# Optimization experiments

Measured on AMD Instinct MI355X. Metric: run time of the kernel, lower is better.

Reference implementation:

```python
import jax, jax.numpy as jnp
import numpy as np
import math
from jax import lax


def quick_gelu(v):
    return v * jax.nn.sigmoid(1.702 * v)


def setup_inputs() -> dict:
    key = jax.random.key(0)
    k0, k1, k2, k3 = jax.random.split(key, 4)
    B, N, C, dim = 64, 1024, 768, 8
    x = jax.random.normal(k0, (B, N, C), dtype=jnp.float32)
    # adapter_down: Linear(C -> dim), xavier-ish init
    Wd = jax.random.normal(k1, (C, dim), dtype=jnp.float32) * (1.0 / math.sqrt(C))
    bd = jnp.zeros((dim,), dtype=jnp.float32)
    # adapter_conv: Conv2d(dim, dim, 3, stride=1, pad=1), HWIO layout
    Wc = jax.random.normal(k2, (3, 3, dim, dim), dtype=jnp.float32) * (1.0 / math.sqrt(9 * dim))
    bc = jnp.zeros((dim,), dtype=jnp.float32)
    # adapter_up: Linear(dim -> C); torch inits this to zeros, but use small
    # random values so the output/gradients are non-trivial for testing.
    Wu = jax.random.normal(k3, (dim, C), dtype=jnp.float32) * 0.02
    bu = jnp.zeros((C,), dtype=jnp.float32)
    return {"x": x, "Wd": Wd, "bd": bd, "Wc": Wc, "bc": bc, "Wu": Wu, "bu": bu}


def reference(x, Wd, bd, Wc, bc, Wu, bu):
    B, N, C = x.shape
    H = int(math.isqrt(N))  # N is a static perfect square (patch grid)
    dim = Wd.shape[1]
    # down projection: [B, N, C] -> [B, N, dim]
    x_down = jnp.einsum("bnc,cd->bnd", x, Wd) + bd
    # reshape to NHWC patch grid, activate, 3x3 same-pad conv
    x_patch = quick_gelu(x_down.reshape(B, H, H, dim))
    x_patch = lax.conv_general_dilated(
        x_patch, Wc, window_strides=(1, 1), padding="SAME",
        dimension_numbers=("NHWC", "HWIO", "NHWC")) + bc
    # flatten back, activate (dropout = identity in eval), up projection
    x_down = quick_gelu(x_patch.reshape(B, N, dim))
    x_up = jnp.einsum("bnd,dc->bnc", x_down, Wu) + bu
    return x_up
```

## Files before the change

### kernel.cpp

```cpp
#include <hip/hip_runtime.h>

#define B_  64
#define N_  1024
#define H_  32
#define C_  768
#define D_  8

__device__ __forceinline__ float qgelu(float v) {
    return v / (1.0f + __expf(-1.702f * v));
}

__device__ __forceinline__ void async_cp16(const float* gp, float* lp) {
    __builtin_amdgcn_global_load_lds(
        (const __attribute__((address_space(1))) void*)gp,
        (__attribute__((address_space(3))) void*)lp, 16, 0, 0);
}

__device__ __forceinline__ void reduce8(float* acc, int lane) {
    {
        const bool hi = lane & 1;
#pragma unroll
        for (int j = 0; j < 4; ++j) {
            const float a = acc[j], b = acc[j + 4];
            acc[j] = hi ? b : a;
            acc[j + 4] = hi ? a : b;
        }
#pragma unroll
        for (int j = 0; j < 4; ++j)
            acc[j] += __shfl_xor(acc[j + 4], 1, 64);
    }
    {
        const bool hi = lane & 2;
#pragma unroll
        for (int j = 0; j < 2; ++j) {
            const float a = acc[j], b = acc[j + 2];
            acc[j] = hi ? b : a;
            acc[j + 2] = hi ? a : b;
        }
#pragma unroll
        for (int j = 0; j < 2; ++j)
            acc[j] += __shfl_xor(acc[j + 2], 2, 64);
    }
    {
        const bool hi = lane & 4;
        const float a = acc[0], b = acc[1];
        acc[0] = hi ? b : a;
        acc[1] = hi ? a : b;
        acc[0] += __shfl_xor(acc[1], 4, 64);
    }
    acc[0] += __shfl_xor(acc[0], 8, 64);
    acc[0] += __shfl_xor(acc[0], 16, 64);
    acc[0] += __shfl_xor(acc[0], 32, 64);
}

__global__ __launch_bounds__(256, 2) void k_down(
    const float* __restrict__ x, const float* __restrict__ Wd,
    const float* __restrict__ bd, float* __restrict__ t1, int nrows)
{
    __shared__ float buf[2][D_ * C_];

    const int wid  = threadIdx.x >> 6;
    const int lane = threadIdx.x & 63;

    for (int i = threadIdx.x; i < D_ * C_; i += 256) {
        const int c = i >> 3, d = i & 7;
        buf[0][d * C_ + c] = Wd[i];
    }
    __syncthreads();
    float4 w[3][D_];
#pragma unroll
    for (int k = 0; k < 3; ++k)
#pragma unroll
        for (int d = 0; d < D_; ++d)
            w[k][d] = *(const float4*)&buf[0][d * C_ + (k * 64 + lane) * 4];
    const int dl = 4 * (lane & 1) + 2 * ((lane >> 1) & 1) + ((lane >> 2) & 1);
    const float bias = bd[dl];
    __syncthreads();

    const int row0 = blockIdx.x * 128;

#define STAGE(T, BUF)                                                        \
    {                                                                        \
        const float* gp0 = x + (size_t)(row0 + (T) * 8) * C_ + wid * 1536;   \
        float* lp0 = &buf[BUF][wid * 1536];                                  \
        _Pragma("unroll")                                                    \
        for (int j = 0; j < 6; ++j)                                          \
            async_cp16(gp0 + j * 256 + lane * 4, lp0 + j * 256);             \
    }

    STAGE(0, 0)
#pragma unroll 1
    for (int t = 0; t < 16; ++t) {
        __syncthreads();
        if (t + 1 < 16) STAGE(t + 1, (t + 1) & 1)

        const float* rowa = &buf[t & 1][(2 * wid) * C_];
        const float* rowb = rowa + C_;
        float a0[D_], a1[D_];
#pragma unroll
        for (int d = 0; d < D_; ++d) { a0[d] = 0.f; a1[d] = 0.f; }
#pragma unroll
        for (int k = 0; k < 3; ++k) {
            const float4 va = *(const float4*)&rowa[(k * 64 + lane) * 4];
            const float4 vb = *(const float4*)&rowb[(k * 64 + lane) * 4];
#pragma unroll
            for (int d = 0; d < D_; ++d) {
                a0[d] += va.x * w[k][d].x + va.y * w[k][d].y
                       + va.z * w[k][d].z + va.w * w[k][d].w;
                a1[d] += vb.x * w[k][d].x + vb.y * w[k][d].y
                       + vb.z * w[k][d].z + vb.w * w[k][d].w;
            }
        }
        reduce8(a0, lane);
        reduce8(a1, lane);

        if (lane < 16) {
            const float s = (lane & 8) ? a1[0] : a0[0];
            const int   r = row0 + t * 8 + 2 * wid + ((lane >> 3) & 1);
            t1[(size_t)r * D_ + dl] = qgelu(s + bias);
        }
        __syncthreads();
    }
#undef STAGE
}

__global__ __launch_bounds__(256, 4) void k_conv(
    const float* __restrict__ t1, const float* __restrict__ Wc,
    const float* __restrict__ bc, float* __restrict__ t2)
{
    __shared__ float sIn[10 * H_ * D_];
    __shared__ float sWc[9 * D_ * D_];
    __shared__ float sbc[D_];

    const int img   = blockIdx.x >> 2;
    const int strip = blockIdx.x & 3;
    const int h0    = strip * 8;
    const float* in = t1 + (size_t)img * N_ * D_;

#pragma unroll
    for (int j = 0; j < 10; ++j) {
        const int i  = threadIdx.x + j * 256;
        const int lr = i >> 8;
        const int rem = i & 255;
        const int g  = h0 - 1 + lr;
        sIn[i] = (g >= 0 && g < H_) ? in[(size_t)g * H_ * D_ + rem] : 0.0f;
    }
    for (int i = threadIdx.x; i < 9 * D_ * D_; i += 256) sWc[i] = Wc[i];
    if (threadIdx.x < D_) sbc[threadIdx.x] = bc[threadIdx.x];
    __syncthreads();

    const int lh = threadIdx.x >> 5;
    const int w  = threadIdx.x & 31;
    float acc[D_];
#pragma unroll
    for (int co = 0; co < D_; ++co) acc[co] = sbc[co];

#pragma unroll
    for (int kh = 0; kh < 3; ++kh) {
        const int lrow = lh + kh;
#pragma unroll
        for (int kw = 0; kw < 3; ++kw) {
            const int ww = w + kw - 1;
            if (ww < 0 || ww >= H_) continue;
            const float* ip = &sIn[(lrow * H_ + ww) * D_];
            const float* wp = &sWc[(kh * 3 + kw) * D_ * D_];
#pragma unroll
            for (int ci = 0; ci < D_; ++ci) {
                const float iv = ip[ci];
#pragma unroll
                for (int co = 0; co < D_; ++co)
                    acc[co] += iv * wp[ci * D_ + co];
            }
        }
    }
    float4 o0, o1;
    o0.x = qgelu(acc[0]); o0.y = qgelu(acc[1]);
    o0.z = qgelu(acc[2]); o0.w = qgelu(acc[3]);
    o1.x = qgelu(acc[4]); o1.y = qgelu(acc[5]);
    o1.z = qgelu(acc[6]); o1.w = qgelu(acc[7]);
    float* tp = t2 + ((size_t)img * N_ + (size_t)(h0 + lh) * H_ + w) * D_;
    *(float4*)tp       = o0;
    *(float4*)(tp + 4) = o1;
}

__global__ __launch_bounds__(256, 3) void k_up(
    const float* __restrict__ t2, const float* __restrict__ Wu,
    const float* __restrict__ bu, float* __restrict__ out, int nrows)
{
    const int wid  = threadIdx.x >> 6;
    const int lane = threadIdx.x & 63;

    float4 w[3][D_];
    float4 bias[3];
#pragma unroll
    for (int j = 0; j < 3; ++j) {
        bias[j] = *(const float4*)&bu[(lane + j * 64) * 4];
#pragma unroll
        for (int d = 0; d < D_; ++d)
            w[j][d] = *(const float4*)&Wu[d * C_ + (lane + j * 64) * 4];
    }

    const int stride = gridDim.x * 4;
    for (int row = blockIdx.x * 4 + wid; row < nrows; row += stride) {
        const float4* rp = (const float4*)(t2 + (size_t)row * D_);
        const float4 ra = rp[0];
        const float4 rb = rp[1];
        const float rv[D_] = { ra.x, ra.y, ra.z, ra.w, rb.x, rb.y, rb.z, rb.w };

#pragma unroll
        for (int j = 0; j < 3; ++j) {
            float4 o = bias[j];
#pragma unroll
            for (int d = 0; d < D_; ++d) {
                o.x += rv[d] * w[j][d].x;
                o.y += rv[d] * w[j][d].y;
                o.z += rv[d] * w[j][d].z;
                o.w += rv[d] * w[j][d].w;
            }
            *(float4*)&out[(size_t)row * C_ + (size_t)(lane + j * 64) * 4] = o;
        }
    }
}

extern "C" void kernel_launch(void* const* d_in, const int* in_sizes, int n_in,
                              void* d_out, int out_size, void* d_ws, size_t ws_size,
                              hipStream_t stream) {
    const float* x  = (const float*)d_in[0];
    const float* Wd = (const float*)d_in[1];
    const float* bd = (const float*)d_in[2];
    const float* Wc = (const float*)d_in[3];
    const float* bc = (const float*)d_in[4];
    const float* Wu = (const float*)d_in[5];
    const float* bu = (const float*)d_in[6];
    float* out = (float*)d_out;

    const int nrows = B_ * N_;
    float* t1 = (float*)d_ws;
    float* t2 = t1 + (size_t)nrows * D_;

    k_down<<<512, 256, 0, stream>>>(x, Wd, bd, t1, nrows);
    k_conv<<<B_ * 4, 256, 0, stream>>>(t1, Wc, bc, t2);
    k_up<<<768, 256, 0, stream>>>(t2, Wu, bu, out, nrows);
}
```

Baseline: 108.2 us.

## Give each wave its own 4-stage async load ring in k_down, removing block barriers

Restructures the down-projection kernel so each wave owns 64 rows and streams them through a private 4-slot LDS ring using async global-to-LDS copies. Fine-grained s_waitcnt vmcnt waits replace the per-iteration block-wide __syncthreads. Results are staged in LDS and written to t1 as coalesced float4 stores at the end. Blocks shrink to 128 threads, so deeper prefetch per wave comes at the cost of fewer waves per block, and correctness depends on the hand-counted vmcnt values.

```diff
diff --git a/kernel.cpp b/kernel.cpp
--- a/kernel.cpp
+++ b/kernel.cpp
@@ -53,75 +53,101 @@
     acc[0] += __shfl_xor(acc[0], 32, 64);
 }
 
-__global__ __launch_bounds__(256, 2) void k_down(
+__global__ __launch_bounds__(128, 2) void k_down(
     const float* __restrict__ x, const float* __restrict__ Wd,
-    const float* __restrict__ bd, float* __restrict__ t1, int nrows)
+    const float* __restrict__ bd, float* __restrict__ t1)
 {
-    __shared__ float buf[2][D_ * C_];
+    __shared__ float ring[2][4][2 * C_];
+    __shared__ float resbuf[2][64 * D_];
+    __shared__ float sbd[D_];
 
     const int wid  = threadIdx.x >> 6;
     const int lane = threadIdx.x & 63;
 
-    for (int i = threadIdx.x; i < D_ * C_; i += 256) {
-        const int c = i >> 3, d = i & 7;
-        buf[0][d * C_ + c] = Wd[i];
+    {
+        float* flat = &ring[0][0][0];
+        for (int i = threadIdx.x; i < D_ * C_; i += 128) {
+            const int c = i >> 3, d = i & 7;
+            flat[d * C_ + c] = Wd[i];
+        }
+        if (threadIdx.x < D_) sbd[threadIdx.x] = bd[threadIdx.x];
     }
     __syncthreads();
     float4 w[3][D_];
-#pragma unroll
-    for (int k = 0; k < 3; ++k)
-#pragma unroll
-        for (int d = 0; d < D_; ++d)
-            w[k][d] = *(const float4*)&buf[0][d * C_ + (k * 64 + lane) * 4];
+    {
+        const float* flat = &ring[0][0][0];
+#pragma unroll
+        for (int k = 0; k < 3; ++k)
+#pragma unroll
+            for (int d = 0; d < D_; ++d)
+                w[k][d] = *(const float4*)&flat[d * C_ + (k * 64 + lane) * 4];
+    }
     const int dl = 4 * (lane & 1) + 2 * ((lane >> 1) & 1) + ((lane >> 2) & 1);
-    const float bias = bd[dl];
+    const float bias = sbd[dl];
     __syncthreads();
 
-    const int row0 = blockIdx.x * 128;
-
-#define STAGE(T, BUF)                                                        \
-    {                                                                        \
-        const float* gp0 = x + (size_t)(row0 + (T) * 8) * C_ + wid * 1536;   \
-        float* lp0 = &buf[BUF][wid * 1536];                                  \
+    const int row0 = (blockIdx.x * 2 + wid) * 64;
+    const float* xw = x + (size_t)row0 * C_;
+    float* myring = &ring[wid][0][0];
+    float* myres  = &resbuf[wid][0];
+
+#define STG(T, S) {                                                          \
+        const float* gp = xw + (size_t)(T) * (2 * C_);                       \
+        float* lp = myring + (S) * (2 * C_);                                 \
         _Pragma("unroll")                                                    \
         for (int j = 0; j < 6; ++j)                                          \
-            async_cp16(gp0 + j * 256 + lane * 4, lp0 + j * 256);             \
-    }
-
-    STAGE(0, 0)
+            async_cp16(gp + j * 256 + lane * 4, lp + j * 256);               \
+    }
+
+#define COMPUTE(T, S) {                                                      \
+        const float* ra = myring + (S) * (2 * C_);                           \
+        const float* rb = ra + C_;                                           \
+        float a0[D_], a1[D_];                                                \
+        _Pragma("unroll")                                                    \
+        for (int d = 0; d < D_; ++d) { a0[d] = 0.f; a1[d] = 0.f; }           \
+        _Pragma("unroll")                                                    \
+        for (int k = 0; k < 3; ++k) {                                        \
+            const float4 va = *(const float4*)&ra[(k * 64 + lane) * 4];      \
+            const float4 vb = *(const float4*)&rb[(k * 64 + lane) * 4];      \
+            _Pragma("unroll")                                                \
+            for (int d = 0; d < D_; ++d) {                                   \
+                a0[d] += va.x*w[k][d].x + va.y*w[k][d].y                     \
+                       + va.z*w[k][d].z + va.w*w[k][d].w;                    \
+                a1[d] += vb.x*w[k][d].x + vb.y*w[k][d].y                     \
+                       + vb.z*w[k][d].z + vb.w*w[k][d].w;                    \
+            }                                                                \
+        }                                                                    \
+        reduce8(a0, lane);                                                   \
+        reduce8(a1, lane);                                                   \
+        if (lane < 16) {                                                     \
+            const float s = (lane & 8) ? a1[0] : a0[0];                      \
+            myres[(2 * (T) + ((lane >> 3) & 1)) * D_ + dl] = qgelu(s + bias);\
+        }                                                                    \
+    }
+
+#define WAITV(N) { asm volatile("s_waitcnt vmcnt(" #N ")" ::: "memory");     \
+                   __builtin_amdgcn_sched_barrier(0); }
+
+    STG(0, 0) STG(1, 1) STG(2, 2)
 #pragma unroll 1
-    for (int t = 0; t < 16; ++t) {
-        __syncthreads();
-        if (t + 1 < 16) STAGE(t + 1, (t + 1) & 1)
-
-        const float* rowa = &buf[t & 1][(2 * wid) * C_];
-        const float* rowb = rowa + C_;
-        float a0[D_], a1[D_];
-#pragma unroll
-        for (int d = 0; d < D_; ++d) { a0[d] = 0.f; a1[d] = 0.f; }
-#pragma unroll
-        for (int k = 0; k < 3; ++k) {
-            const float4 va = *(const float4*)&rowa[(k * 64 + lane) * 4];
-            const float4 vb = *(const float4*)&rowb[(k * 64 + lane) * 4];
-#pragma unroll
-            for (int d = 0; d < D_; ++d) {
-                a0[d] += va.x * w[k][d].x + va.y * w[k][d].y
-                       + va.z * w[k][d].z + va.w * w[k][d].w;
-                a1[d] += vb.x * w[k][d].x + vb.y * w[k][d].y
-                       + vb.z * w[k][d].z + vb.w * w[k][d].w;
-            }
-        }
-        reduce8(a0, lane);
-        reduce8(a1, lane);
-
-        if (lane < 16) {
-            const float s = (lane & 8) ? a1[0] : a0[0];
-            const int   r = row0 + t * 8 + 2 * wid + ((lane >> 3) & 1);
-            t1[(size_t)r * D_ + dl] = qgelu(s + bias);
-        }
-        __syncthreads();
-    }
-#undef STAGE
+    for (int t = 0; t < 29; ++t) {
+        STG(t + 3, (t + 3) & 3)
+        WAITV(18)
+        COMPUTE(t, t & 3)
+    }
+    WAITV(12) COMPUTE(29, 1)
+    WAITV(6)  COMPUTE(30, 2)
+    WAITV(0)  COMPUTE(31, 3)
+
+#pragma unroll
+    for (int j = 0; j < 2; ++j) {
+        const int i4 = j * 64 + lane;
+        const float4 v = *(const float4*)&myres[i4 * 4];
+        *(float4*)&t1[(size_t)row0 * D_ + (size_t)i4 * 4] = v;
+    }
+#undef STG
+#undef COMPUTE
+#undef WAITV
 }
 
 __global__ __launch_bounds__(256, 4) void k_conv(
@@ -238,7 +264,7 @@
     float* t1 = (float*)d_ws;
     float* t2 = t1 + (size_t)nrows * D_;
 
-    k_down<<<512, 256, 0, stream>>>(x, Wd, bd, t1, nrows);
+    k_down<<<512, 128, 0, stream>>>(x, Wd, bd, t1);
     k_conv<<<B_ * 4, 256, 0, stream>>>(t1, Wc, bc, t2);
     k_up<<<768, 256, 0, stream>>>(t2, Wu, bu, out, nrows);
 }
```

Measured after the change: 115.1 us. +6.4%, slower.
